# Kernel tuning notes

Hardware: AMD Instinct MI355X
Metric: run time of the kernel (lower is better)

Reference implementation:

```python
import jax, jax.numpy as jnp
import numpy as np

EPS = 1e-10      # normalizer eps from the torch module
IN_EPS = 1e-5    # torch InstanceNorm2d default eps
STRIDE = 2
PAD = 1


def _dw_conv_transpose(x, W):
    """Depthwise ConvTranspose2d applied for every output channel at once.

    x: [B, Cin, H, W]
    W: [Cin, Cout, kh, kw]  (W[:, i] is sub_convs[i].weight of shape [Cin, 1, kh, kw])
    returns: [B, Cin, Cout, H', W'] where channel (c, i) = convT of x[:, c] with W[c, i].
    """
    Cin, Cout, kh, kw = W.shape
    # Transposed conv == dilated conv with spatially flipped kernel,
    # lhs_dilation = stride, padding = k - 1 - pad (output_padding = 0).
    rhs = jnp.flip(W, axis=(-2, -1)).reshape(Cin * Cout, 1, kh, kw)
    pad_h = (kh - 1 - PAD, kh - 1 - PAD)
    pad_w = (kw - 1 - PAD, kw - 1 - PAD)
    out = jax.lax.conv_general_dilated(
        x, rhs,
        window_strides=(1, 1),
        padding=(pad_h, pad_w),
        lhs_dilation=(STRIDE, STRIDE),
        dimension_numbers=('NCHW', 'OIHW', 'NCHW'),
        feature_group_count=Cin,
    )  # [B, Cin*Cout, H', W'], group-major: group c -> channels c*Cout:(c+1)*Cout
    B = x.shape[0]
    return out.reshape(B, Cin, Cout, out.shape[2], out.shape[3])


def setup_inputs() -> dict:
    key = jax.random.key(0)
    k1, k2, k3 = jax.random.split(key, 3)
    B, Cin, Cout, H, Wd, K = 2, 64, 64, 48, 48, 4
    x = jax.random.normal(k1, (B, Cin, H, Wd), dtype=jnp.float32)
    # Positive-leaning weights keep the normalizer (convT of ones) away from zero.
    W = 0.05 + 0.1 * jax.random.uniform(k2, (Cin, Cout, K, K), dtype=jnp.float32)
    bias = 0.02 * jax.random.normal(k3, (Cout,), dtype=jnp.float32)
    return {"x": x, "W": W, "bias": bias}


def reference(x, W, bias):
    # numerator: depthwise convT of the input for every (in_ch, out_ch) pair
    num = _dw_conv_transpose(x, W)                       # [B, Cin, Cout, H', W']
    # normalizer: same convT applied to ones (batch-independent -> batch of 1)
    den = _dw_conv_transpose(jnp.ones_like(x[:1]), W) + EPS  # [1, Cin, Cout, H', W']
    out = jnp.sum(num / den, axis=1) + bias[None, :, None, None]  # [B, Cout, H', W']
    # InstanceNorm2d (no affine, biased variance) over spatial dims per (b, c)
    mean = jnp.mean(out, axis=(2, 3), keepdims=True)
    var = jnp.var(out, axis=(2, 3), keepdims=True)
    return (out - mean) / jnp.sqrt(var + IN_EPS)
```

## Files before the change

### kernel.cpp

```cpp
#include <hip/hip_runtime.h>

#define BB    2
#define CIN   64
#define NI    64
#define HIN   48
#define WIN   48
#define HO    96
#define WO    96
#define EPSN  1e-10f
#define IN_EPS 1e-5f
#define IMG   (HO*WO)
#define NIMG  (BB*NI)

template <int CS>
__global__ __launch_bounds__(256) void conv_kernel(
        const float* __restrict__ x, const float* __restrict__ Wt,
        float* __restrict__ part) {
    constexpr int NC = CIN / CS;
    const int bi = blockIdx.x, s = blockIdx.y;
    const int b = bi >> 6, i = bi & 63, c0 = s * NC;
    const int tid = threadIdx.x;
    const int ty = tid >> 4, tx = tid & 15;

    __shared__ __align__(16) float sF[NC * 16];
    __shared__ float sW[NC * 16];
    __shared__ float sR[NC * 16];
    __shared__ float sFix[384];

    for (int e = tid; e < NC * 16; e += 256) {
        const int c = e >> 4, j = e & 15;
        const float* wp = Wt + ((size_t)(c0 + c) * NI + i) * 16;
        sW[e] = wp[j];
        const int py = (j >> 3) & 1, px = (j >> 2) & 1, a = (j >> 1) & 1, bb = j & 1;
        const int kh = py ? (a ? 2 : 0) : (a ? 3 : 1);
        const int kw = px ? (bb ? 2 : 0) : (bb ? 3 : 1);
        const int r0 = py ? 0 : 1, r1 = py ? 2 : 3;
        const int q0 = px ? 0 : 1, q1 = px ? 2 : 3;
        const float den = wp[r0 * 4 + q0] + wp[r0 * 4 + q1]
                        + wp[r1 * 4 + q0] + wp[r1 * 4 + q1];
        sF[e] = wp[kh * 4 + kw] / (den + EPSN);
        const int cy = j >> 2, cx = j & 3;
        const int THn[4] = {1, 2, 2, 1};
        const int THv[4][2] = {{1, 1}, {0, 2}, {1, 3}, {2, 2}};
        float den2 = 0.f;
        for (int aa = 0; aa < THn[cy]; ++aa)
            for (int bb2 = 0; bb2 < THn[cx]; ++bb2)
                den2 += wp[THv[cy][aa] * 4 + THv[cx][bb2]];
        sR[e] = 1.f / (den2 + EPSN);
    }
    __syncthreads();

    int rowOff[5], colIdx[5];
    bool rOk[5], cOk[5];
#pragma unroll
    for (int rr = 0; rr < 5; ++rr) {
        const int r = 3 * ty + rr - 1;
        rOk[rr] = (unsigned)r < (unsigned)HIN;
        rowOff[rr] = (rOk[rr] ? r : 0) * WIN;
    }
#pragma unroll
    for (int cc = 0; cc < 5; ++cc) {
        const int cI = 3 * tx + cc - 1;
        cOk[cc] = (unsigned)cI < (unsigned)WIN;
        colIdx[cc] = cOk[cc] ? cI : 0;
    }

    float acc[6][6];
#pragma unroll
    for (int r = 0; r < 6; ++r)
#pragma unroll
        for (int j = 0; j < 6; ++j) acc[r][j] = 0.f;

    const float* xb = x + ((size_t)b * CIN + c0) * (HIN * WIN);

#pragma unroll 2
    for (int c = 0; c < NC; ++c) {
        float g[16];
        const float4* gf = (const float4*)&sF[c * 16];
#pragma unroll
        for (int q = 0; q < 4; ++q) {
            const float4 t = gf[q];
            g[4 * q] = t.x; g[4 * q + 1] = t.y; g[4 * q + 2] = t.z; g[4 * q + 3] = t.w;
        }

        const float* xc = xb + c * (HIN * WIN);
        float xv[5][5];
#pragma unroll
        for (int rr = 0; rr < 5; ++rr)
#pragma unroll
            for (int cc = 0; cc < 5; ++cc) {
                const float v = xc[rowOff[rr] + colIdx[cc]];
                xv[rr][cc] = (rOk[rr] & cOk[cc]) ? v : 0.f;
            }

#pragma unroll
        for (int r = 0; r < 6; ++r) {
            const int rhi = (r + 3) >> 1, rlo = rhi - 1, py = r & 1;
#pragma unroll
            for (int j = 0; j < 6; ++j) {
                const int chi = (j + 3) >> 1, clo = chi - 1, px = j & 1;
                const float* gg = &g[py * 8 + px * 4];
                acc[r][j] += xv[rhi][chi] * gg[0] + xv[rhi][clo] * gg[1]
                           + xv[rlo][chi] * gg[2] + xv[rlo][clo] * gg[3];
            }
        }
    }

    for (int p = tid; p < 380; p += 256) {
        int y, xo;
        if (p < 96)       { y = 0;            xo = p; }
        else if (p < 192) { y = 95;           xo = p - 96; }
        else if (p < 286) { y = p - 192 + 1;  xo = 0; }
        else              { y = p - 286 + 1;  xo = 95; }
        const int hA = (y + 1) >> 1, hB = hA - 1;
        const int khA = (y & 1) ? 0 : 1, khB = khA + 2;
        const int wA = (xo + 1) >> 1, wB = wA - 1;
        const int kwA = (xo & 1) ? 0 : 1, kwB = kwA + 2;
        const bool okA = hA < HIN, okB = hB >= 0;
        const bool okC = wA < WIN, okD = wB >= 0;
        const int hAc = okA ? hA : 0, hBc = okB ? hB : 0;
        const int wAc = okC ? wA : 0, wBc = okD ? wB : 0;
        const int cy = (y == 0) ? 0 : (y == 95) ? 3 : ((y & 1) ? 1 : 2);
        const int cx = (xo == 0) ? 0 : (xo == 95) ? 3 : ((xo & 1) ? 1 : 2);
        const int cls = cy * 4 + cx;
        float v = 0.f;
        for (int c = 0; c < NC; ++c) {
            const float* xc = xb + c * (HIN * WIN);
            const float* wc = &sW[c * 16];
            float num = 0.f;
            if (okA & okC) num += xc[hAc * WIN + wAc] * wc[khA * 4 + kwA];
            if (okA & okD) num += xc[hAc * WIN + wBc] * wc[khA * 4 + kwB];
            if (okB & okC) num += xc[hBc * WIN + wAc] * wc[khB * 4 + kwA];
            if (okB & okD) num += xc[hBc * WIN + wBc] * wc[khB * 4 + kwB];
            v += num * sR[c * 16 + cls];
        }
        sFix[p] = v;
    }
    __syncthreads();

#pragma unroll
    for (int r = 0; r < 6; ++r)
#pragma unroll
        for (int j = 0; j < 6; ++j) {
            const int y = 6 * ty + r, xo = 6 * tx + j;
            if (y == 0)        acc[r][j] = sFix[xo];
            else if (y == 95)  acc[r][j] = sFix[96 + xo];
            else if (xo == 0)  acc[r][j] = sFix[192 + y - 1];
            else if (xo == 95) acc[r][j] = sFix[286 + y - 1];
        }

    float* pp = part + ((size_t)s * NIMG + bi) * IMG + (6 * ty) * WO + 6 * tx;
#pragma unroll
    for (int r = 0; r < 6; ++r)
#pragma unroll
        for (int jj = 0; jj < 3; ++jj) {
            float2 v;
            v.x = acc[r][2 * jj];
            v.y = acc[r][2 * jj + 1];
            *(float2*)(pp + r * WO + 2 * jj) = v;
        }
}

template <int CS>
__global__ __launch_bounds__(256) void reduce_stats_kernel(
        const float* __restrict__ part, const float* __restrict__ bias,
        float* __restrict__ sumimg, float2* __restrict__ pairs) {
    const int slice = blockIdx.x, bi = blockIdx.y;
    const int tid = threadIdx.x;
    const float bv = bias[bi & 63];
    const float4* pb = (const float4*)part + (size_t)bi * (IMG / 4);
    const size_t stride4 = (size_t)NIMG * (IMG / 4);
    float4* sb = (float4*)sumimg + (size_t)bi * (IMG / 4);

    float s1 = 0.f, s2 = 0.f;
#pragma unroll
    for (int k = 0; k < 3; ++k) {
        const int idx = slice * 768 + k * 256 + tid;
        float4 t = pb[idx];
#pragma unroll
        for (int s = 1; s < CS; ++s) {
            const float4 q = pb[s * stride4 + idx];
            t.x += q.x; t.y += q.y; t.z += q.z; t.w += q.w;
        }
        t.x += bv; t.y += bv; t.z += bv; t.w += bv;
        sb[idx] = t;
        s1 += t.x + t.y + t.z + t.w;
        s2 += t.x * t.x + t.y * t.y + t.z * t.z + t.w * t.w;
    }

    __shared__ float red[8];
#pragma unroll
    for (int off = 32; off > 0; off >>= 1) {
        s1 += __shfl_down(s1, off, 64);
        s2 += __shfl_down(s2, off, 64);
    }
    if ((tid & 63) == 0) { red[tid >> 6] = s1; red[4 + (tid >> 6)] = s2; }
    __syncthreads();
    if (tid == 0)
        pairs[bi * 3 + slice] = make_float2(red[0] + red[1] + red[2] + red[3],
                                            red[4] + red[5] + red[6] + red[7]);
}

__global__ __launch_bounds__(256) void normalize_kernel(
        const float* __restrict__ sumimg, const float2* __restrict__ pairs,
        float* __restrict__ out) {
    const int slice = blockIdx.x, bi = blockIdx.y;
    const int tid = threadIdx.x;
    const float2 p0 = pairs[bi * 3 + 0], p1 = pairs[bi * 3 + 1], p2 = pairs[bi * 3 + 2];
    const float mean = (p0.x + p1.x + p2.x) * (1.f / 9216.f);
    const float m2   = (p0.y + p1.y + p2.y) * (1.f / 9216.f);
    const float inv  = rsqrtf(m2 - mean * mean + IN_EPS);
    const float4* sb = (const float4*)sumimg + (size_t)bi * (IMG / 4);
    float4* ob = (float4*)out + (size_t)bi * (IMG / 4);
#pragma unroll
    for (int k = 0; k < 3; ++k) {
        const int idx = slice * 768 + k * 256 + tid;
        float4 t = sb[idx];
        t.x = (t.x - mean) * inv; t.y = (t.y - mean) * inv;
        t.z = (t.z - mean) * inv; t.w = (t.w - mean) * inv;
        ob[idx] = t;
    }
}

extern "C" void kernel_launch(void* const* d_in, const int* in_sizes, int n_in,
                              void* d_out, int out_size, void* d_ws, size_t ws_size,
                              hipStream_t stream) {
    const float* x    = (const float*)d_in[0];
    const float* Wt   = (const float*)d_in[1];
    const float* bias = (const float*)d_in[2];
    float* out = (float*)d_out;
    float* ws  = (float*)d_ws;

    const size_t need4 = ((size_t)4 * NIMG * IMG + (size_t)NIMG * IMG + NIMG * 6) * 4;
    if (ws_size >= need4) {
        float* part   = ws;
        float* sumimg = ws + (size_t)4 * NIMG * IMG;
        float2* pairs = (float2*)(ws + (size_t)5 * NIMG * IMG);
        conv_kernel<4><<<dim3(NIMG, 4), 256, 0, stream>>>(x, Wt, part);
        reduce_stats_kernel<4><<<dim3(3, NIMG), 256, 0, stream>>>(part, bias, sumimg, pairs);
        normalize_kernel<<<dim3(3, NIMG), 256, 0, stream>>>(sumimg, pairs, out);
    } else {
        float2* pairs = (float2*)ws;
        conv_kernel<1><<<dim3(NIMG, 1), 256, 0, stream>>>(x, Wt, out);
        reduce_stats_kernel<1><<<dim3(3, NIMG), 256, 0, stream>>>(out, bias, out, pairs);
        normalize_kernel<<<dim3(3, NIMG), 256, 0, stream>>>(out, pairs, out);
    }
}
```

Baseline: 105.3 us.

## Pre-pad input to drop conv bounds checks and fuse stats with normalize

Adds a pad kernel that writes a zero-bordered copy of x, so the conv inner loop loads a 5x5 window without per-element bounds predicates or clamped indices. The reduce-stats and normalize kernels are merged into one 768-thread block per image. That block keeps the summed values in registers and computes mean and inverse std in shared memory, removing the sumimg round trip and one launch. It costs an extra launch and a padded copy of the input, and each image's epilogue now runs on only 128 blocks.

```diff
diff --git a/kernel.cpp b/kernel.cpp
--- a/kernel.cpp
+++ b/kernel.cpp
@@ -11,10 +11,27 @@
 #define IN_EPS 1e-5f
 #define IMG   (HO*WO)
 #define NIMG  (BB*NI)
+#define PH    50
+#define PW    52
+#define XPN   (BB*CIN*PH*PW)
+
+__global__ __launch_bounds__(256) void pad_kernel(const float* __restrict__ x,
+                                                  float* __restrict__ xpad) {
+    const int slice = blockIdx.x >> 1, half = blockIdx.x & 1;
+    const float* xs = x + (size_t)slice * (HIN * WIN);
+    float* xd = xpad + (size_t)slice * (PH * PW) + half * 25 * PW;
+    for (int e = threadIdx.x; e < 25 * PW; e += 256) {
+        const int rp = e / PW, pc = e - rp * PW;
+        const int h = half * 25 + rp - 1, w = pc - 1;
+        float v = 0.f;
+        if ((unsigned)h < HIN && (unsigned)w < WIN) v = xs[h * WIN + w];
+        xd[e] = v;
+    }
+}
 
 template <int CS>
 __global__ __launch_bounds__(256) void conv_kernel(
-        const float* __restrict__ x, const float* __restrict__ Wt,
+        const float* __restrict__ xpad, const float* __restrict__ Wt,
         float* __restrict__ part) {
     constexpr int NC = CIN / CS;
     const int bi = blockIdx.x, s = blockIdx.y;
@@ -50,28 +67,13 @@
     }
     __syncthreads();
 
-    int rowOff[5], colIdx[5];
-    bool rOk[5], cOk[5];
-#pragma unroll
-    for (int rr = 0; rr < 5; ++rr) {
-        const int r = 3 * ty + rr - 1;
-        rOk[rr] = (unsigned)r < (unsigned)HIN;
-        rowOff[rr] = (rOk[rr] ? r : 0) * WIN;
-    }
-#pragma unroll
-    for (int cc = 0; cc < 5; ++cc) {
-        const int cI = 3 * tx + cc - 1;
-        cOk[cc] = (unsigned)cI < (unsigned)WIN;
-        colIdx[cc] = cOk[cc] ? cI : 0;
-    }
-
     float acc[6][6];
 #pragma unroll
     for (int r = 0; r < 6; ++r)
 #pragma unroll
         for (int j = 0; j < 6; ++j) acc[r][j] = 0.f;
 
-    const float* xb = x + ((size_t)b * CIN + c0) * (HIN * WIN);
+    const float* xb = xpad + ((size_t)b * CIN + c0) * (PH * PW) + (3 * ty) * PW + 3 * tx;
 
 #pragma unroll 2
     for (int c = 0; c < NC; ++c) {
@@ -83,15 +85,12 @@
             g[4 * q] = t.x; g[4 * q + 1] = t.y; g[4 * q + 2] = t.z; g[4 * q + 3] = t.w;
         }
 
-        const float* xc = xb + c * (HIN * WIN);
+        const float* xc = xb + c * (PH * PW);
         float xv[5][5];
 #pragma unroll
         for (int rr = 0; rr < 5; ++rr)
 #pragma unroll
-            for (int cc = 0; cc < 5; ++cc) {
-                const float v = xc[rowOff[rr] + colIdx[cc]];
-                xv[rr][cc] = (rOk[rr] & cOk[cc]) ? v : 0.f;
-            }
+            for (int cc = 0; cc < 5; ++cc) xv[rr][cc] = xc[rr * PW + cc];
 
 #pragma unroll
         for (int r = 0; r < 6; ++r) {
@@ -106,6 +105,7 @@
         }
     }
 
+    const float* xb2 = xpad + ((size_t)b * CIN + c0) * (PH * PW);
     for (int p = tid; p < 380; p += 256) {
         int y, xo;
         if (p < 96)       { y = 0;            xo = p; }
@@ -116,22 +116,18 @@
         const int khA = (y & 1) ? 0 : 1, khB = khA + 2;
         const int wA = (xo + 1) >> 1, wB = wA - 1;
         const int kwA = (xo & 1) ? 0 : 1, kwB = kwA + 2;
-        const bool okA = hA < HIN, okB = hB >= 0;
-        const bool okC = wA < WIN, okD = wB >= 0;
-        const int hAc = okA ? hA : 0, hBc = okB ? hB : 0;
-        const int wAc = okC ? wA : 0, wBc = okD ? wB : 0;
         const int cy = (y == 0) ? 0 : (y == 95) ? 3 : ((y & 1) ? 1 : 2);
         const int cx = (xo == 0) ? 0 : (xo == 95) ? 3 : ((xo & 1) ? 1 : 2);
         const int cls = cy * 4 + cx;
+        const int rA = (hA + 1) * PW, rB = (hB + 1) * PW;
         float v = 0.f;
         for (int c = 0; c < NC; ++c) {
-            const float* xc = xb + c * (HIN * WIN);
+            const float* xc = xb2 + c * (PH * PW);
             const float* wc = &sW[c * 16];
-            float num = 0.f;
-            if (okA & okC) num += xc[hAc * WIN + wAc] * wc[khA * 4 + kwA];
-            if (okA & okD) num += xc[hAc * WIN + wBc] * wc[khA * 4 + kwB];
-            if (okB & okC) num += xc[hBc * WIN + wAc] * wc[khB * 4 + kwA];
-            if (okB & okD) num += xc[hBc * WIN + wBc] * wc[khB * 4 + kwB];
+            const float num = xc[rA + wA + 1] * wc[khA * 4 + kwA]
+                            + xc[rA + wB + 1] * wc[khA * 4 + kwB]
+                            + xc[rB + wA + 1] * wc[khB * 4 + kwA]
+                            + xc[rB + wB + 1] * wc[khB * 4 + kwB];
             v += num * sR[c * 16 + cls];
         }
         sFix[p] = v;
@@ -162,20 +158,20 @@
 }
 
 template <int CS>
-__global__ __launch_bounds__(256) void reduce_stats_kernel(
+__global__ __launch_bounds__(768) void epilogue_kernel(
         const float* __restrict__ part, const float* __restrict__ bias,
-        float* __restrict__ sumimg, float2* __restrict__ pairs) {
-    const int slice = blockIdx.x, bi = blockIdx.y;
+        float* __restrict__ out) {
+    const int bi = blockIdx.x;
     const int tid = threadIdx.x;
     const float bv = bias[bi & 63];
     const float4* pb = (const float4*)part + (size_t)bi * (IMG / 4);
     const size_t stride4 = (size_t)NIMG * (IMG / 4);
-    float4* sb = (float4*)sumimg + (size_t)bi * (IMG / 4);
-
+
+    float4 v[3];
     float s1 = 0.f, s2 = 0.f;
 #pragma unroll
     for (int k = 0; k < 3; ++k) {
-        const int idx = slice * 768 + k * 256 + tid;
+        const int idx = k * 768 + tid;
         float4 t = pb[idx];
 #pragma unroll
         for (int s = 1; s < CS; ++s) {
@@ -183,39 +179,38 @@
             t.x += q.x; t.y += q.y; t.z += q.z; t.w += q.w;
         }
         t.x += bv; t.y += bv; t.z += bv; t.w += bv;
-        sb[idx] = t;
+        v[k] = t;
         s1 += t.x + t.y + t.z + t.w;
         s2 += t.x * t.x + t.y * t.y + t.z * t.z + t.w * t.w;
     }
 
-    __shared__ float red[8];
+    __shared__ float red[24];
+    __shared__ float stat[2];
 #pragma unroll
     for (int off = 32; off > 0; off >>= 1) {
         s1 += __shfl_down(s1, off, 64);
         s2 += __shfl_down(s2, off, 64);
     }
-    if ((tid & 63) == 0) { red[tid >> 6] = s1; red[4 + (tid >> 6)] = s2; }
-    __syncthreads();
-    if (tid == 0)
-        pairs[bi * 3 + slice] = make_float2(red[0] + red[1] + red[2] + red[3],
-                                            red[4] + red[5] + red[6] + red[7]);
-}
-
-__global__ __launch_bounds__(256) void normalize_kernel(
-        const float* __restrict__ sumimg, const float2* __restrict__ pairs,
-        float* __restrict__ out) {
-    const int slice = blockIdx.x, bi = blockIdx.y;
-    const int tid = threadIdx.x;
-    const float2 p0 = pairs[bi * 3 + 0], p1 = pairs[bi * 3 + 1], p2 = pairs[bi * 3 + 2];
-    const float mean = (p0.x + p1.x + p2.x) * (1.f / 9216.f);
-    const float m2   = (p0.y + p1.y + p2.y) * (1.f / 9216.f);
-    const float inv  = rsqrtf(m2 - mean * mean + IN_EPS);
-    const float4* sb = (const float4*)sumimg + (size_t)bi * (IMG / 4);
+    const int w = tid >> 6;
+    if ((tid & 63) == 0) { red[w] = s1; red[12 + w] = s2; }
+    __syncthreads();
+    if (tid == 0) {
+        float t1 = 0.f, t2 = 0.f;
+#pragma unroll
+        for (int k = 0; k < 12; ++k) { t1 += red[k]; t2 += red[12 + k]; }
+        const float mean = t1 * (1.f / 9216.f);
+        const float m2 = t2 * (1.f / 9216.f);
+        stat[0] = mean;
+        stat[1] = rsqrtf(m2 - mean * mean + IN_EPS);
+    }
+    __syncthreads();
+    const float mean = stat[0], inv = stat[1];
+
     float4* ob = (float4*)out + (size_t)bi * (IMG / 4);
 #pragma unroll
     for (int k = 0; k < 3; ++k) {
-        const int idx = slice * 768 + k * 256 + tid;
-        float4 t = sb[idx];
+        const int idx = k * 768 + tid;
+        float4 t = v[k];
         t.x = (t.x - mean) * inv; t.y = (t.y - mean) * inv;
         t.z = (t.z - mean) * inv; t.w = (t.w - mean) * inv;
         ob[idx] = t;
@@ -231,18 +226,16 @@
     float* out = (float*)d_out;
     float* ws  = (float*)d_ws;
 
-    const size_t need4 = ((size_t)4 * NIMG * IMG + (size_t)NIMG * IMG + NIMG * 6) * 4;
+    float* xpad = ws;
+    pad_kernel<<<BB * CIN * 2, 256, 0, stream>>>(x, xpad);
+
+    const size_t need4 = ((size_t)XPN + (size_t)4 * NIMG * IMG) * 4;
     if (ws_size >= need4) {
-        float* part   = ws;
-        float* sumimg = ws + (size_t)4 * NIMG * IMG;
-        float2* pairs = (float2*)(ws + (size_t)5 * NIMG * IMG);
-        conv_kernel<4><<<dim3(NIMG, 4), 256, 0, stream>>>(x, Wt, part);
-        reduce_stats_kernel<4><<<dim3(3, NIMG), 256, 0, stream>>>(part, bias, sumimg, pairs);
-        normalize_kernel<<<dim3(3, NIMG), 256, 0, stream>>>(sumimg, pairs, out);
+        float* part = ws + XPN;
+        conv_kernel<4><<<dim3(NIMG, 4), 256, 0, stream>>>(xpad, Wt, part);
+        epilogue_kernel<4><<<NIMG, 768, 0, stream>>>(part, bias, out);
     } else {
-        float2* pairs = (float2*)ws;
-        conv_kernel<1><<<dim3(NIMG, 1), 256, 0, stream>>>(x, Wt, out);
-        reduce_stats_kernel<1><<<dim3(3, NIMG), 256, 0, stream>>>(out, bias, out, pairs);
-        normalize_kernel<<<dim3(3, NIMG), 256, 0, stream>>>(out, pairs, out);
-    }
-}
+        conv_kernel<1><<<dim3(NIMG, 1), 256, 0, stream>>>(xpad, Wt, out);
+        epilogue_kernel<1><<<NIMG, 768, 0, stream>>>(out, bias, out);
+    }
+}
```

New measurement: 96.68 us. 1.09x faster.
